# Kernel optimization log

Measured on AMD Instinct MI355X. Metric: run time of the kernel, lower is better.

The kernel has to match this reference:

```python
import jax, jax.numpy as jnp
import numpy as np


def setup_inputs() -> dict:
    key = jax.random.key(0)
    ks = jax.random.split(key, 8)
    B, N, M, H = 8192, 2048, 2048, 10
    return {
        "X": jax.random.normal(ks[0], (B, N), dtype=jnp.float32),
        "weight": jax.random.normal(ks[1], (N, M), dtype=jnp.float32),
        "W1": jax.random.normal(ks[2], (3, H), dtype=jnp.float32) * 0.5,
        "b1": jax.random.normal(ks[3], (H,), dtype=jnp.float32) * 0.1,
        "W2": jax.random.normal(ks[4], (H, H), dtype=jnp.float32) * 0.3,
        "b2": jax.random.normal(ks[5], (H,), dtype=jnp.float32) * 0.1,
        "W3": jax.random.normal(ks[6], (H, 1), dtype=jnp.float32) * 0.3,
        "b3": jax.random.normal(ks[7], (1,), dtype=jnp.float32) * 0.1,
    }


def reference(X, weight, W1, b1, W2, b2, W3, b3):
    # NCA local rule, vectorized over all (i, j) cells.
    # 'forward'  = mean of column j excluding row i  (leave-one-out col mean)
    # 'backward' = mean of row i excluding column j  (leave-one-out row mean)
    n, m = weight.shape
    col_sum = jnp.sum(weight, axis=0, keepdims=True)            # [1, m]
    row_sum = jnp.sum(weight, axis=1, keepdims=True)            # [n, 1]
    fwd_mean = (col_sum - weight) / jnp.float32(n - 1)          # [n, m]
    bwd_mean = (row_sum - weight) / jnp.float32(m - 1)          # [n, m]
    feats = jnp.stack([weight, fwd_mean, bwd_mean], axis=-1)    # [n, m, 3]
    # tiny 3 -> 10 -> 10 -> 1 MLP applied per cell
    h = jax.nn.relu(feats @ W1 + b1)                            # [n, m, 10]
    h = jax.nn.relu(h @ W2 + b2)                                # [n, m, 10]
    updates = (h @ W3 + b3)[..., 0]                             # [n, m]
    new_weight = weight + updates
    # forward: softmax(X @ W)
    return jax.nn.softmax(X @ new_weight, axis=-1)
```

## Files before the change

### kernel.cpp

```cpp
#include <hip/hip_runtime.h>
#include <hip/hip_bf16.h>


typedef int int4v __attribute__((ext_vector_type(4)));
typedef int int16v __attribute__((ext_vector_type(16)));

#define GK 2048
#define NROWS 2048
#define MCOLS 2048
#define NCHUNK 16

#define CS_BLOCKS 128
#define RS_BLOCKS 2048
__global__ __launch_bounds__(256) void pre_kernel(
    const float* __restrict__ X, const float* __restrict__ W,
    signed char* __restrict__ X1, signed char* __restrict__ X2,
    float* __restrict__ sx1,
    float* __restrict__ part, float* __restrict__ rowS) {
  const int bid = blockIdx.x;
  const int tid = threadIdx.x;

  if (bid < CS_BLOCKS) {
    int chunk = bid >> 3;
    int j = (bid & 7) * 256 + tid;
    int i0 = chunk * (NROWS / NCHUNK);
    float s = 0.f;
    for (int i = i0; i < i0 + NROWS / NCHUNK; ++i) s += W[(size_t)i * MCOLS + j];
    part[(size_t)chunk * MCOLS + j] = s;
    return;
  }
  if (bid < CS_BLOCKS + RS_BLOCKS) {
    int row = bid - CS_BLOCKS;
    const float4* p = (const float4*)(W + (size_t)row * MCOLS);
    float4 a = p[tid];
    float4 b = p[tid + 256];
    float v = (a.x + a.y) + (a.z + a.w) + (b.x + b.y) + (b.z + b.w);
    __shared__ float red[256];
    red[tid] = v;
    __syncthreads();
    for (int s = 128; s > 0; s >>= 1) {
      if (tid < s) red[tid] += red[tid + s];
      __syncthreads();
    }
    if (tid == 0) rowS[row] = red[0];
    return;
  }
  {
    int rb = bid - CS_BLOCKS - RS_BLOCKS;
    const int lane = tid & 63, wv = tid >> 6;
    const int row = rb * 4 + wv;
    const float4* xr = (const float4*)(X + (size_t)row * GK) + lane * 8;
    float xs[32];
#pragma unroll
    for (int i = 0; i < 8; ++i) {
      float4 t = xr[i];
      xs[i * 4 + 0] = t.x; xs[i * 4 + 1] = t.y;
      xs[i * 4 + 2] = t.z; xs[i * 4 + 3] = t.w;
    }
    float am = 0.f;
#pragma unroll
    for (int i = 0; i < 32; ++i) am = fmaxf(am, fabsf(xs[i]));
#pragma unroll
    for (int off = 32; off > 0; off >>= 1)
      am = fmaxf(am, __shfl_xor(am, off));
    float s1 = am * (1.0f / 127.0f);
    float inv = 127.0f / am;
    unsigned w1[8], w2[8];
#pragma unroll
    for (int i = 0; i < 8; ++i) { w1[i] = 0u; w2[i] = 0u; }
#pragma unroll
    for (int i = 0; i < 32; ++i) {
      int q1 = (int)rintf(xs[i] * inv);
      float r = xs[i] - (float)q1 * s1;
      int q2 = (int)rintf(r * (254.0f * inv));
      w1[i >> 2] |= (unsigned)(q1 & 255) << ((i & 3) * 8);
      w2[i >> 2] |= (unsigned)(q2 & 255) << ((i & 3) * 8);
    }
    const int m32 = row >> 5, ml = row & 31;
    int4v* d1 = (int4v*)X1 + ((size_t)m32 * 64 + lane) * 64;
    int4v* d2 = (int4v*)X2 + ((size_t)m32 * 64 + lane) * 64;
    int4v v1lo = {(int)w1[0], (int)w1[1], (int)w1[2], (int)w1[3]};
    int4v v1hi = {(int)w1[4], (int)w1[5], (int)w1[6], (int)w1[7]};
    int4v v2lo = {(int)w2[0], (int)w2[1], (int)w2[2], (int)w2[3]};
    int4v v2hi = {(int)w2[4], (int)w2[5], (int)w2[6], (int)w2[7]};
    d1[ml]      = v1lo;
    d1[ml + 32] = v1hi;
    d2[ml]      = v2lo;
    d2[ml + 32] = v2hi;
    if (lane == 0) sx1[row] = s1;
  }
}

__global__ __launch_bounds__(256) void nca_update_kernel(
    const float* __restrict__ W, const float* __restrict__ part,
    const float* __restrict__ rowS,
    const float* __restrict__ W1, const float* __restrict__ b1,
    const float* __restrict__ W2, const float* __restrict__ b2,
    const float* __restrict__ W3, const float* __restrict__ b3,
    float* __restrict__ Wt) {
  __shared__ float sColS[32];
  __shared__ float cred[NCHUNK][33];
  __shared__ float Tf[32][33];
  const int tid = threadIdx.x;
  const int i0 = blockIdx.y * 32;
  const int j0 = blockIdx.x * 32;

  {
    int ch = tid >> 5;
    int jl = tid & 31;
    cred[ch][jl]     = part[(size_t)ch * MCOLS + j0 + jl];
    cred[ch + 8][jl] = part[(size_t)(ch + 8) * MCOLS + j0 + jl];
  }
  __syncthreads();
  if (tid < 32) {
    float s = 0.f;
#pragma unroll
    for (int c = 0; c < NCHUNK; ++c) s += cred[c][tid];
    sColS[tid] = s;
  }
  __syncthreads();

  const int r = tid >> 5;
  const int c = tid & 31;

  float w[4], fwd[4], bwd[4];
#pragma unroll
  for (int cell = 0; cell < 4; ++cell) {
    int il = r + 8 * cell;
    float wv = W[(size_t)(i0 + il) * MCOLS + j0 + c];
    w[cell] = wv;
    fwd[cell] = (sColS[c] - wv) * (1.0f / (float)(NROWS - 1));
    bwd[cell] = (rowS[i0 + il] - wv) * (1.0f / (float)(MCOLS - 1));
  }

  float h1[4][10];
#pragma unroll
  for (int o = 0; o < 10; ++o) {
    float w1a = W1[o], w1b = W1[10 + o], w1c = W1[20 + o], bb = b1[o];
#pragma unroll
    for (int cell = 0; cell < 4; ++cell) {
      float v = fmaf(w[cell], w1a, fmaf(fwd[cell], w1b, fmaf(bwd[cell], w1c, bb)));
      h1[cell][o] = fmaxf(v, 0.f);
    }
  }
  const float b3v = b3[0];
  float u[4] = {b3v, b3v, b3v, b3v};
#pragma unroll
  for (int o = 0; o < 10; ++o) {
    float h2[4];
    float bb = b2[o];
#pragma unroll
    for (int cell = 0; cell < 4; ++cell) h2[cell] = bb;
#pragma unroll
    for (int p = 0; p < 10; ++p) {
      float wv = W2[p * 10 + o];
#pragma unroll
      for (int cell = 0; cell < 4; ++cell) h2[cell] = fmaf(h1[cell][p], wv, h2[cell]);
    }
    float w3 = W3[o];
#pragma unroll
    for (int cell = 0; cell < 4; ++cell) u[cell] = fmaf(fmaxf(h2[cell], 0.f), w3, u[cell]);
  }

#pragma unroll
  for (int cell = 0; cell < 4; ++cell) {
    int il = r + 8 * cell;
    Tf[il][c] = w[cell] + u[cell];
  }
  __syncthreads();

  {
    int r2 = tid >> 4;
    int ic = (tid & 15) * 2;
#pragma unroll
    for (int half = 0; half < 2; ++half) {
      int jl = r2 + 16 * half;
      float2 v = make_float2(Tf[ic][jl], Tf[ic + 1][jl]);
      *(float2*)(&Wt[(size_t)(j0 + jl) * NROWS + i0 + ic]) = v;
    }
  }
}

__global__ __launch_bounds__(256) void bquant_kernel(
    const float* __restrict__ Wt, signed char* __restrict__ B1,
    signed char* __restrict__ B2, float* __restrict__ sw1) {
  const int tid = threadIdx.x;
  const int lane = tid & 63, wv = tid >> 6;
  const int row = blockIdx.x * 4 + wv;
  const float4* wr = (const float4*)(Wt + (size_t)row * GK) + lane * 8;
  float xs[32];
#pragma unroll
  for (int i = 0; i < 8; ++i) {
    float4 t = wr[i];
    xs[i * 4 + 0] = t.x; xs[i * 4 + 1] = t.y;
    xs[i * 4 + 2] = t.z; xs[i * 4 + 3] = t.w;
  }
  float am = 0.f;
#pragma unroll
  for (int i = 0; i < 32; ++i) am = fmaxf(am, fabsf(xs[i]));
#pragma unroll
  for (int off = 32; off > 0; off >>= 1)
    am = fmaxf(am, __shfl_xor(am, off));
  float s1 = am * (1.0f / 127.0f);
  float inv = 127.0f / am;
  unsigned w1[8], w2[8];
#pragma unroll
  for (int i = 0; i < 8; ++i) { w1[i] = 0u; w2[i] = 0u; }
#pragma unroll
  for (int i = 0; i < 32; ++i) {
    int q1 = (int)rintf(xs[i] * inv);
    float r = xs[i] - (float)q1 * s1;
    int q2 = (int)rintf(r * (254.0f * inv));
    w1[i >> 2] |= (unsigned)(q1 & 255) << ((i & 3) * 8);
    w2[i >> 2] |= (unsigned)(q2 & 255) << ((i & 3) * 8);
  }
  const int n32 = row >> 5, nl = row & 31;
  int4v* d1 = (int4v*)B1 + ((size_t)n32 * 64 + lane) * 64;
  int4v* d2 = (int4v*)B2 + ((size_t)n32 * 64 + lane) * 64;
  int4v v1lo = {(int)w1[0], (int)w1[1], (int)w1[2], (int)w1[3]};
  int4v v1hi = {(int)w1[4], (int)w1[5], (int)w1[6], (int)w1[7]};
  int4v v2lo = {(int)w2[0], (int)w2[1], (int)w2[2], (int)w2[3]};
  int4v v2hi = {(int)w2[4], (int)w2[5], (int)w2[6], (int)w2[7]};
  d1[nl]      = v1lo;
  d1[nl + 32] = v1hi;
  d2[nl]      = v2lo;
  d2[nl + 32] = v2hi;
  if (lane == 0) sw1[row] = s1;
}

#define BM 256
#define BN 128

#define MFMA_I8 __builtin_amdgcn_mfma_i32_32x32x32_i8

#define LOADT(S, k)                                                            \
  S##a1_0 = A1p[a0 + (size_t)(k) * 64];                                        \
  S##a1_1 = A1p[a1 + (size_t)(k) * 64];                                        \
  S##a2_0 = A2p[a0 + (size_t)(k) * 64];                                        \
  S##a2_1 = A2p[a1 + (size_t)(k) * 64];                                        \
  S##b1_0 = B1p[b0 + (size_t)(k) * 64];                                        \
  S##b1_1 = B1p[b1 + (size_t)(k) * 64];                                        \
  S##b2_0 = B2p[b0 + (size_t)(k) * 64];                                        \
  S##b2_1 = B2p[b1 + (size_t)(k) * 64];

#define MM12S(S)                                                               \
  acc_h[0][0] = MFMA_I8(S##a1_0, S##b1_0, acc_h[0][0], 0, 0, 0);               \
  acc_h[0][1] = MFMA_I8(S##a1_0, S##b1_1, acc_h[0][1], 0, 0, 0);               \
  acc_h[1][0] = MFMA_I8(S##a1_1, S##b1_0, acc_h[1][0], 0, 0, 0);               \
  acc_h[1][1] = MFMA_I8(S##a1_1, S##b1_1, acc_h[1][1], 0, 0, 0);               \
  acc_c[0][0] = MFMA_I8(S##a1_0, S##b2_0, acc_c[0][0], 0, 0, 0);               \
  acc_c[0][1] = MFMA_I8(S##a1_0, S##b2_1, acc_c[0][1], 0, 0, 0);               \
  acc_c[1][0] = MFMA_I8(S##a1_1, S##b2_0, acc_c[1][0], 0, 0, 0);               \
  acc_c[1][1] = MFMA_I8(S##a1_1, S##b2_1, acc_c[1][1], 0, 0, 0);               \
  acc_c[0][0] = MFMA_I8(S##a2_0, S##b1_0, acc_c[0][0], 0, 0, 0);               \
  acc_c[0][1] = MFMA_I8(S##a2_0, S##b1_1, acc_c[0][1], 0, 0, 0);               \
  acc_c[1][0] = MFMA_I8(S##a2_1, S##b1_0, acc_c[1][0], 0, 0, 0);               \
  acc_c[1][1] = MFMA_I8(S##a2_1, S##b1_1, acc_c[1][1], 0, 0, 0);

__global__ __launch_bounds__(512, 2) void gemm_kernel(
    const int4v* __restrict__ A1p, const int4v* __restrict__ A2p,
    const int4v* __restrict__ B1p, const int4v* __restrict__ B2p,
    const float* __restrict__ sw1, float* __restrict__ C) {
  const int tid = threadIdx.x;
  const int lane = tid & 63;
  const int wave = tid >> 6;
  const int wr = wave >> 1;
  const int wc = wave & 1;

  const int bx = blockIdx.x;
  const int by = blockIdx.y;

  const size_t a0 = ((size_t)(by * 8 + wr * 2 + 0) * 64) * 64 + lane;
  const size_t a1 = ((size_t)(by * 8 + wr * 2 + 1) * 64) * 64 + lane;
  const size_t b0 = ((size_t)(bx * 4 + wc * 2 + 0) * 64) * 64 + lane;
  const size_t b1 = ((size_t)(bx * 4 + wc * 2 + 1) * 64) * 64 + lane;

  int16v acc_h[2][2], acc_c[2][2];
#pragma unroll
  for (int i = 0; i < 2; ++i)
#pragma unroll
    for (int j = 0; j < 2; ++j)
#pragma unroll
      for (int e = 0; e < 16; ++e) { acc_h[i][j][e] = 0; acc_c[i][j][e] = 0; }

  int4v Pa1_0, Pa1_1, Pa2_0, Pa2_1, Pb1_0, Pb1_1, Pb2_0, Pb2_1;
  int4v Qa1_0, Qa1_1, Qa2_0, Qa2_1, Qb1_0, Qb1_1, Qb2_0, Qb2_1;

  LOADT(P, 0);
#pragma unroll 1
  for (int k = 0; k < 62; k += 2) {
    LOADT(Q, k + 1);
    MM12S(P);
    LOADT(P, k + 2);
    MM12S(Q);
  }
  LOADT(Q, 63);
  MM12S(P);
  MM12S(Q);

  const int ecol = lane & 31;
  const int erow = 4 * (lane >> 5);
#pragma unroll
  for (int ni = 0; ni < 2; ++ni) {
    int col = bx * BN + wc * 64 + ni * 32 + ecol;
    float sw = sw1[col];
#pragma unroll
    for (int mi = 0; mi < 2; ++mi) {
#pragma unroll
      for (int reg = 0; reg < 16; ++reg) {
        int row = by * BM + wr * 64 + mi * 32 + (reg & 3) + 8 * (reg >> 2) + erow;
        float v = (float)acc_h[mi][ni][reg] + (float)acc_c[mi][ni][reg] * (1.0f / 254.0f);
        C[(size_t)row * MCOLS + col] = v * sw;
      }
    }
  }
}

__global__ __launch_bounds__(256) void softmax_kernel(
    float* __restrict__ C, const float* __restrict__ sx1) {
  const int lane = threadIdx.x & 63;
  const int wv = threadIdx.x >> 6;
  const int row = blockIdx.x * 4 + wv;
  const float sx = sx1[row];
  float4* p = (float4*)(C + (size_t)row * MCOLS);

  float4 v[8];
#pragma unroll
  for (int j = 0; j < 8; ++j) {
    v[j] = p[j * 64 + lane];
    v[j].x *= sx; v[j].y *= sx; v[j].z *= sx; v[j].w *= sx;
  }

  float vmax = -3.4e38f;
#pragma unroll
  for (int j = 0; j < 8; ++j)
    vmax = fmaxf(vmax, fmaxf(fmaxf(v[j].x, v[j].y), fmaxf(v[j].z, v[j].w)));
#pragma unroll
  for (int off = 32; off > 0; off >>= 1)
    vmax = fmaxf(vmax, __shfl_xor(vmax, off));

  float sum = 0.f;
#pragma unroll
  for (int j = 0; j < 8; ++j) {
    v[j].x = __expf(v[j].x - vmax);
    v[j].y = __expf(v[j].y - vmax);
    v[j].z = __expf(v[j].z - vmax);
    v[j].w = __expf(v[j].w - vmax);
    sum += (v[j].x + v[j].y) + (v[j].z + v[j].w);
  }
#pragma unroll
  for (int off = 32; off > 0; off >>= 1)
    sum += __shfl_xor(sum, off);
  float inv = 1.0f / sum;

#pragma unroll
  for (int j = 0; j < 8; ++j) {
    v[j].x *= inv; v[j].y *= inv; v[j].z *= inv; v[j].w *= inv;
    p[j * 64 + lane] = v[j];
  }
}

extern "C" void kernel_launch(void* const* d_in, const int* in_sizes, int n_in,
                              void* d_out, int out_size, void* d_ws, size_t ws_size,
                              hipStream_t stream) {
  const float* X      = (const float*)d_in[0];
  const float* weight = (const float*)d_in[1];
  const float* W1     = (const float*)d_in[2];
  const float* b1     = (const float*)d_in[3];
  const float* W2     = (const float*)d_in[4];
  const float* b2     = (const float*)d_in[5];
  const float* W3     = (const float*)d_in[6];
  const float* b3     = (const float*)d_in[7];
  float* out = (float*)d_out;

  const int N = 2048, M = 2048;
  const int Bdim = in_sizes[0] / N;

  float* rowS = (float*)d_ws;
  float* part = rowS + 2048;
  float* sx1  = part + NCHUNK * 2048;
  float* sw1  = sx1 + 8192;
  float* Wt   = sw1 + 2048;
  signed char* X1 = (signed char*)(Wt + (size_t)M * N);
  signed char* X2 = X1 + (size_t)Bdim * N;
  signed char* B1q = X2 + (size_t)Bdim * N;
  signed char* B2q = B1q + (size_t)M * N;

  pre_kernel<<<CS_BLOCKS + RS_BLOCKS + Bdim / 4, 256, 0, stream>>>(
      X, weight, X1, X2, sx1, part, rowS);

  nca_update_kernel<<<dim3(M / 32, N / 32), 256, 0, stream>>>(
      weight, part, rowS, W1, b1, W2, b2, W3, b3, Wt);

  bquant_kernel<<<M / 4, 256, 0, stream>>>(Wt, B1q, B2q, sw1);

  gemm_kernel<<<dim3(M / BN, Bdim / BM), 512, 0, stream>>>(
      (const int4v*)X1, (const int4v*)X2, (const int4v*)B1q, (const int4v*)B2q,
      sw1, out);

  softmax_kernel<<<Bdim / 4, 256, 0, stream>>>(out, sx1);
}
```

Measured before the change: 325.6 us.

## Coalesce int8 quantized stores via LDS transpose and interleave GEMM loads with MFMAs

The quantization kernels for X and the weight now stage each wave's packed int8 rows in shared memory. After a barrier they write them out so that four consecutive rows land contiguously in the MFMA-tiled layout, replacing the old scattered 16-byte stores. In the GEMM main loop, sched_group_barrier hints interleave vector memory loads with MFMA instructions to overlap them better. The cost is an extra LDS round trip and barrier in the prep kernels. The scheduling hints may also constrain the compiler in ways that hurt.

New measurement: 303.8 us. 1.07x faster.

```diff
diff --git a/kernel.cpp b/kernel.cpp
--- a/kernel.cpp
+++ b/kernel.cpp
@@ -76,18 +76,26 @@
       w1[i >> 2] |= (unsigned)(q1 & 255) << ((i & 3) * 8);
       w2[i >> 2] |= (unsigned)(q2 & 255) << ((i & 3) * 8);
     }
-    const int m32 = row >> 5, ml = row & 31;
-    int4v* d1 = (int4v*)X1 + ((size_t)m32 * 64 + lane) * 64;
-    int4v* d2 = (int4v*)X2 + ((size_t)m32 * 64 + lane) * 64;
     int4v v1lo = {(int)w1[0], (int)w1[1], (int)w1[2], (int)w1[3]};
     int4v v1hi = {(int)w1[4], (int)w1[5], (int)w1[6], (int)w1[7]};
     int4v v2lo = {(int)w2[0], (int)w2[1], (int)w2[2], (int)w2[3]};
     int4v v2hi = {(int)w2[4], (int)w2[5], (int)w2[6], (int)w2[7]};
-    d1[ml]      = v1lo;
-    d1[ml + 32] = v1hi;
-    d2[ml]      = v2lo;
-    d2[ml + 32] = v2hi;
+    __shared__ int4v tr[4][2][2][65];
+    tr[wv][0][0][lane] = v1lo;
+    tr[wv][0][1][lane] = v1hi;
+    tr[wv][1][0][lane] = v2lo;
+    tr[wv][1][1][lane] = v2hi;
     if (lane == 0) sx1[row] = s1;
+    __syncthreads();
+    const int k = tid >> 2, r = tid & 3;
+    const int m32 = rb >> 3;
+    const int ml0 = (rb * 4) & 31;
+    int4v* d1 = (int4v*)X1 + ((size_t)m32 * 64 + k) * 64;
+    int4v* d2 = (int4v*)X2 + ((size_t)m32 * 64 + k) * 64;
+    d1[ml0 + r]      = tr[r][0][0][k];
+    d1[ml0 + r + 32] = tr[r][0][1][k];
+    d2[ml0 + r]      = tr[r][1][0][k];
+    d2[ml0 + r + 32] = tr[r][1][1][k];
   }
 }
 
@@ -186,7 +194,8 @@
     signed char* __restrict__ B2, float* __restrict__ sw1) {
   const int tid = threadIdx.x;
   const int lane = tid & 63, wv = tid >> 6;
-  const int row = blockIdx.x * 4 + wv;
+  const int rb = blockIdx.x;
+  const int row = rb * 4 + wv;
   const float4* wr = (const float4*)(Wt + (size_t)row * GK) + lane * 8;
   float xs[32];
 #pragma unroll
@@ -214,18 +223,26 @@
     w1[i >> 2] |= (unsigned)(q1 & 255) << ((i & 3) * 8);
     w2[i >> 2] |= (unsigned)(q2 & 255) << ((i & 3) * 8);
   }
-  const int n32 = row >> 5, nl = row & 31;
-  int4v* d1 = (int4v*)B1 + ((size_t)n32 * 64 + lane) * 64;
-  int4v* d2 = (int4v*)B2 + ((size_t)n32 * 64 + lane) * 64;
   int4v v1lo = {(int)w1[0], (int)w1[1], (int)w1[2], (int)w1[3]};
   int4v v1hi = {(int)w1[4], (int)w1[5], (int)w1[6], (int)w1[7]};
   int4v v2lo = {(int)w2[0], (int)w2[1], (int)w2[2], (int)w2[3]};
   int4v v2hi = {(int)w2[4], (int)w2[5], (int)w2[6], (int)w2[7]};
-  d1[nl]      = v1lo;
-  d1[nl + 32] = v1hi;
-  d2[nl]      = v2lo;
-  d2[nl + 32] = v2hi;
+  __shared__ int4v tr[4][2][2][65];
+  tr[wv][0][0][lane] = v1lo;
+  tr[wv][0][1][lane] = v1hi;
+  tr[wv][1][0][lane] = v2lo;
+  tr[wv][1][1][lane] = v2hi;
   if (lane == 0) sw1[row] = s1;
+  __syncthreads();
+  const int k = tid >> 2, r = tid & 3;
+  const int n32 = rb >> 3;
+  const int nl0 = (rb * 4) & 31;
+  int4v* d1 = (int4v*)B1 + ((size_t)n32 * 64 + k) * 64;
+  int4v* d2 = (int4v*)B2 + ((size_t)n32 * 64 + k) * 64;
+  d1[nl0 + r]      = tr[r][0][0][k];
+  d1[nl0 + r + 32] = tr[r][0][1][k];
+  d2[nl0 + r]      = tr[r][1][0][k];
+  d2[nl0 + r + 32] = tr[r][1][1][k];
 }
 
 #define BM 256
@@ -257,6 +274,13 @@
   acc_c[1][0] = MFMA_I8(S##a2_1, S##b1_0, acc_c[1][0], 0, 0, 0);               \
   acc_c[1][1] = MFMA_I8(S##a2_1, S##b1_1, acc_c[1][1], 0, 0, 0);
 
+#define SGB_PATTERN                                                            \
+  _Pragma("unroll")                                                            \
+  for (int _g = 0; _g < 8; ++_g) {                                             \
+    __builtin_amdgcn_sched_group_barrier(0x020, 2, 0);          \
+    __builtin_amdgcn_sched_group_barrier(0x008, 3, 0);          \
+  }
+
 __global__ __launch_bounds__(512, 2) void gemm_kernel(
     const int4v* __restrict__ A1p, const int4v* __restrict__ A2p,
     const int4v* __restrict__ B1p, const int4v* __restrict__ B2p,
@@ -293,6 +317,7 @@
     MM12S(P);
     LOADT(P, k + 2);
     MM12S(Q);
+    SGB_PATTERN;
   }
   LOADT(Q, 63);
   MM12S(P);
```
